# Performance work log

Hardware: AMD Instinct MI355X
Metric: run time of the kernel (lower is better)

Reference implementation:

```python
import jax, jax.numpy as jnp
import numpy as np

N_NODES = 100000


def _gat_conv(x, edge_index, W, att_src, att_dst, bias, concat):
    """PyG-style GATConv (eval mode, self-loops already in edge_index).
    x: [N, F_in], W: [F_in, H*C], att_*: [H, C], bias: [H*C] or [C].
    """
    N = x.shape[0]
    H, C = att_src.shape
    xl = (x @ W).reshape(N, H, C)                      # [N, H, C]
    a_src = jnp.einsum('nhc,hc->nh', xl, att_src)      # [N, H]
    a_dst = jnp.einsum('nhc,hc->nh', xl, att_dst)      # [N, H]
    src, dst = edge_index[0], edge_index[1]
    e = jax.nn.leaky_relu(a_src[src] + a_dst[dst], negative_slope=0.2)  # [E, H]
    # segment softmax over incoming edges per destination node
    e_max = jax.ops.segment_max(e, dst, num_segments=N)                 # [N, H]
    e_exp = jnp.exp(e - e_max[dst])                                     # [E, H]
    denom = jax.ops.segment_sum(e_exp, dst, num_segments=N)             # [N, H]
    alpha = e_exp / (denom[dst] + 1e-16)                                # [E, H]
    msg = xl[src] * alpha[:, :, None]                                   # [E, H, C]
    out = jax.ops.segment_sum(msg, dst, num_segments=N)                 # [N, H, C]
    out = out.reshape(N, H * C) if concat else out.mean(axis=1)
    return out + bias


def setup_inputs() -> dict:
    key = jax.random.key(0)
    ks = jax.random.split(key, 12)
    in_dim, hidden, heads, out_dim = 128, 16, 8, 64
    E = 1600000
    x = jax.random.normal(ks[0], (N_NODES, in_dim), dtype=jnp.float32)
    edge_index = jax.random.randint(ks[1], (2, E), 0, N_NODES, dtype=jnp.int32)
    s1 = 1.0 / np.sqrt(in_dim)
    s2 = 1.0 / np.sqrt(hidden * heads)
    return {
        'x': x,
        'edge_index': edge_index,
        'W1': jax.random.normal(ks[2], (in_dim, heads * hidden), dtype=jnp.float32) * s1,
        'att_src1': jax.random.normal(ks[3], (heads, hidden), dtype=jnp.float32) * 0.1,
        'att_dst1': jax.random.normal(ks[4], (heads, hidden), dtype=jnp.float32) * 0.1,
        'b1': jnp.zeros((heads * hidden,), dtype=jnp.float32),
        'W2': jax.random.normal(ks[5], (heads * hidden, out_dim), dtype=jnp.float32) * s2,
        'att_src2': jax.random.normal(ks[6], (1, out_dim), dtype=jnp.float32) * 0.1,
        'att_dst2': jax.random.normal(ks[7], (1, out_dim), dtype=jnp.float32) * 0.1,
        'b2': jnp.zeros((out_dim,), dtype=jnp.float32),
    }


def reference(x, edge_index, W1, att_src1, att_dst1, b1, W2, att_src2, att_dst2, b2):
    N = x.shape[0]
    # PyG GATConv default add_self_loops=True
    loops = jnp.tile(jnp.arange(N, dtype=edge_index.dtype), (2, 1))
    ei = jnp.concatenate([edge_index, loops], axis=1)
    h = _gat_conv(x, ei, W1, att_src1, att_dst1, b1, concat=True)
    h = jax.nn.elu(h)
    # dropout is identity in eval mode
    out = _gat_conv(h, ei, W2, att_src2, att_dst2, b2, concat=False)
    return out
```

## Files before the change

kernel.cpp:

```cpp
#include <hip/hip_runtime.h>
#include <cmath>

typedef _Float16 half8 __attribute__((ext_vector_type(8)));
typedef float f32x4 __attribute__((ext_vector_type(4)));

#define CAP 48

__device__ __forceinline__ float elu1(float v) {
    return v > 0.f ? v : (__expf(v) - 1.f);
}

__global__ __launch_bounds__(256) void k_gemm1(
    const float* __restrict__ x, const float* __restrict__ W,
    const float* __restrict__ att_s, const float* __restrict__ att_d,
    _Float16* __restrict__ xlh, float* __restrict__ a_s, float* __restrict__ a_d,
    int* __restrict__ cnt, int N)
{
    __shared__ _Float16 Wt[128 * 136];
    int t = threadIdx.x;

    for (int i = blockIdx.x * 256 + t; i < N; i += gridDim.x * 256) cnt[i] = 0;

    for (int i = t; i < 128 * 128; i += 256) {
        int k = i >> 7, n = i & 127;
        Wt[n * 136 + k] = (_Float16)W[i];
    }
    __syncthreads();

    int wave = t >> 6, lane = t & 63;
    int cl = lane & 15, quad = lane >> 4;
    int arow = blockIdx.x * 64 + wave * 16 + cl;
    int rr = arow < N ? arow : N - 1;

    half8 af[4];
#pragma unroll
    for (int ks = 0; ks < 4; ks++) {
        const float4* p = (const float4*)(x + (size_t)rr * 128 + ks * 32 + quad * 8);
        float4 A = p[0], B = p[1];
        af[ks][0] = (_Float16)A.x; af[ks][1] = (_Float16)A.y;
        af[ks][2] = (_Float16)A.z; af[ks][3] = (_Float16)A.w;
        af[ks][4] = (_Float16)B.x; af[ks][5] = (_Float16)B.y;
        af[ks][6] = (_Float16)B.z; af[ks][7] = (_Float16)B.w;
    }

    f32x4 acc[8];
#pragma unroll
    for (int nt = 0; nt < 8; nt++) acc[nt] = (f32x4){0.f, 0.f, 0.f, 0.f};

#pragma unroll
    for (int nt = 0; nt < 8; nt++) {
        int n = nt * 16 + cl;
#pragma unroll
        for (int ks = 0; ks < 4; ks++) {
            half8 bf = *(const half8*)&Wt[n * 136 + ks * 32 + quad * 8];
            acc[nt] = __builtin_amdgcn_mfma_f32_16x16x32_f16(af[ks], bf, acc[nt], 0, 0, 0);
        }
    }

    float asl[8], adl[8];
#pragma unroll
    for (int nt = 0; nt < 8; nt++) {
        asl[nt] = att_s[nt * 16 + cl];
        adl[nt] = att_d[nt * 16 + cl];
    }

    int rbase = blockIdx.x * 64 + wave * 16 + quad * 4;
#pragma unroll
    for (int r = 0; r < 4; r++) {
        int orow = rbase + r;
        bool ok = orow < N;
#pragma unroll
        for (int nt = 0; nt < 8; nt++) {
            float v = acc[nt][r];
            if (ok) xlh[(size_t)orow * 128 + nt * 16 + cl] = (_Float16)v;
        }
#pragma unroll
        for (int nt = 0; nt < 8; nt++) {
            float ps = acc[nt][r] * asl[nt];
            float pd = acc[nt][r] * adl[nt];
            ps += __shfl_xor(ps, 1); ps += __shfl_xor(ps, 2);
            ps += __shfl_xor(ps, 4); ps += __shfl_xor(ps, 8);
            pd += __shfl_xor(pd, 1); pd += __shfl_xor(pd, 2);
            pd += __shfl_xor(pd, 4); pd += __shfl_xor(pd, 8);
            if (ok && cl == 0) {
                a_s[(size_t)orow * 8 + nt] = ps;
                a_d[(size_t)orow * 8 + nt] = pd;
            }
        }
    }
}

__global__ __launch_bounds__(256) void k_scatter(
    const int* __restrict__ src, const int* __restrict__ dst,
    int* __restrict__ cnt, int* __restrict__ sorted, int E, int M, int npc)
{
    int color = blockIdx.x & 7;
    int lo = color * npc, hi = lo + npc;
    int nb = gridDim.x >> 3;
    size_t stride = (size_t)nb * 256;
    for (size_t e = (size_t)(blockIdx.x >> 3) * 256 + threadIdx.x; e < (size_t)M; e += stride) {
        int s, d;
        if (e < (size_t)E) { s = src[e]; d = dst[e]; } else { s = (int)(e - E); d = s; }
        if (d >= lo && d < hi) {
            int pos = atomicAdd(&cnt[d], 1);
            if (pos < CAP) sorted[(size_t)d * CAP + pos] = s;
        }
    }
}

__global__ __launch_bounds__(256) void k_agg1_gemm2(
    const int* __restrict__ cnt, const int* __restrict__ ss,
    const float* __restrict__ as, const float* __restrict__ ad,
    const _Float16* __restrict__ xlh, const float* __restrict__ b1,
    const float* __restrict__ W2,
    const float* __restrict__ att_s2, const float* __restrict__ att_d2,
    _Float16* __restrict__ xl2h, float* __restrict__ a_s2, float* __restrict__ a_d2, int N)
{
    __shared__ _Float16 W2t[64 * 136];
    __shared__ _Float16 Ht[32 * 136];
    __shared__ float asb[2][32], adb[2][32];

    int t = threadIdx.x;

    for (int i = t; i < 128 * 64; i += 256) {
        int k = i >> 6, n = i & 63;
        W2t[n * 136 + k] = (_Float16)W2[i];
    }

    int ln = t >> 3;
    int g = blockIdx.x * 32 + ln;
    int lane8 = t & 7;
    int c = lane8 * 16;
    {
        int gg = g < N ? g : N - 1;
        int deg = cnt[gg]; deg = deg < CAP ? deg : CAP;
        int start = gg * CAP, end = start + deg;
        float adv = ad[(size_t)gg * 8 + lane8];

        float l = 0.f;
        float acc[16];
#pragma unroll
        for (int j = 0; j < 16; j++) acc[j] = 0.f;

        int i = start;
        for (; i + 2 <= end; i += 2) {
            int s0 = ss[i], s1 = ss[i + 1];
            float a0 = as[(size_t)s0 * 8 + lane8];
            float a1 = as[(size_t)s1 * 8 + lane8];
            const _Float16* p0 = xlh + (size_t)s0 * 128 + c;
            const _Float16* p1 = xlh + (size_t)s1 * 128 + c;
            half8 x0a = *(const half8*)p0, x0b = *(const half8*)(p0 + 8);
            half8 x1a = *(const half8*)p1, x1b = *(const half8*)(p1 + 8);
            float v0 = a0 + adv; v0 = v0 > 0.f ? v0 : 0.2f * v0;
            float v1 = a1 + adv; v1 = v1 > 0.f ? v1 : 0.2f * v1;
            float w0 = __expf(v0), w1 = __expf(v1);
            l += w0 + w1;
#pragma unroll
            for (int j = 0; j < 8; j++) {
                acc[j]     += (float)x0a[j] * w0 + (float)x1a[j] * w1;
                acc[j + 8] += (float)x0b[j] * w0 + (float)x1b[j] * w1;
            }
        }
        if (i < end) {
            int s0 = ss[i];
            float v0 = as[(size_t)s0 * 8 + lane8] + adv;
            v0 = v0 > 0.f ? v0 : 0.2f * v0;
            float w0 = __expf(v0);
            l += w0;
            const _Float16* p0 = xlh + (size_t)s0 * 128 + c;
            half8 x0a = *(const half8*)p0, x0b = *(const half8*)(p0 + 8);
#pragma unroll
            for (int j = 0; j < 8; j++) {
                acc[j]     += (float)x0a[j] * w0;
                acc[j + 8] += (float)x0b[j] * w0;
            }
        }
        float inv = 1.f / (l + 1e-16f);
        float4 bq[4];
        bq[0] = *(const float4*)(b1 + c);
        bq[1] = *(const float4*)(b1 + c + 4);
        bq[2] = *(const float4*)(b1 + c + 8);
        bq[3] = *(const float4*)(b1 + c + 12);
        const float* bb = (const float*)bq;
        half8 o0, o1;
#pragma unroll
        for (int j = 0; j < 8; j++) {
            o0[j] = (_Float16)elu1(acc[j] * inv + bb[j]);
            o1[j] = (_Float16)elu1(acc[j + 8] * inv + bb[j + 8]);
        }
        *(half8*)&Ht[ln * 136 + c] = o0;
        *(half8*)&Ht[ln * 136 + c + 8] = o1;
    }
    __syncthreads();

    int wave = t >> 6, lane = t & 63;
    int cl = lane & 15, quad = lane >> 4;
    int rt = wave >> 1;
    int half = wave & 1;

    half8 af[4];
#pragma unroll
    for (int ks = 0; ks < 4; ks++)
        af[ks] = *(const half8*)&Ht[(rt * 16 + cl) * 136 + ks * 32 + quad * 8];

    f32x4 acc2[2];
    acc2[0] = (f32x4){0.f, 0.f, 0.f, 0.f};
    acc2[1] = (f32x4){0.f, 0.f, 0.f, 0.f};
    float asl[2], adl[2];
#pragma unroll
    for (int ntl = 0; ntl < 2; ntl++) {
        int n = (half * 2 + ntl) * 16 + cl;
        asl[ntl] = att_s2[n];
        adl[ntl] = att_d2[n];
#pragma unroll
        for (int ks = 0; ks < 4; ks++) {
            half8 bf = *(const half8*)&W2t[n * 136 + ks * 32 + quad * 8];
            acc2[ntl] = __builtin_amdgcn_mfma_f32_16x16x32_f16(af[ks], bf, acc2[ntl], 0, 0, 0);
        }
    }

#pragma unroll
    for (int r = 0; r < 4; r++) {
        int lrow = rt * 16 + quad * 4 + r;
        int orow = blockIdx.x * 32 + lrow;
        bool ok = orow < N;
        float ps = 0.f, pd = 0.f;
#pragma unroll
        for (int ntl = 0; ntl < 2; ntl++) {
            float v = acc2[ntl][r];
            if (ok) xl2h[(size_t)orow * 64 + (half * 2 + ntl) * 16 + cl] = (_Float16)v;
            ps += v * asl[ntl];
            pd += v * adl[ntl];
        }
        ps += __shfl_xor(ps, 1); ps += __shfl_xor(ps, 2);
        ps += __shfl_xor(ps, 4); ps += __shfl_xor(ps, 8);
        pd += __shfl_xor(pd, 1); pd += __shfl_xor(pd, 2);
        pd += __shfl_xor(pd, 4); pd += __shfl_xor(pd, 8);
        if (cl == 0) { asb[half][lrow] = ps; adb[half][lrow] = pd; }
    }
    __syncthreads();
    if (t < 32) {
        int orow = blockIdx.x * 32 + t;
        if (orow < N) {
            a_s2[orow] = asb[0][t] + asb[1][t];
            a_d2[orow] = adb[0][t] + adb[1][t];
        }
    }
}

__global__ __launch_bounds__(256) void k_agg2(
    const int* __restrict__ cnt, const int* __restrict__ ss,
    const float* __restrict__ as, const float* __restrict__ ad,
    const _Float16* __restrict__ xlh, const float* __restrict__ b2,
    float* __restrict__ out, int N)
{
    int t = threadIdx.x;
    int g = (blockIdx.x * 256 + t) >> 3;
    if (g >= N) return;
    int lane = t & 7;
    int c = lane * 8;
    int deg = cnt[g]; deg = deg < CAP ? deg : CAP;
    int start = g * CAP, end = start + deg;
    float adv = ad[g];

    float l = 0.f;
    float acc[8];
#pragma unroll
    for (int j = 0; j < 8; j++) acc[j] = 0.f;

    int i = start;
    for (; i + 4 <= end; i += 4) {
        int s0 = ss[i], s1 = ss[i + 1], s2 = ss[i + 2], s3 = ss[i + 3];
        float a0 = as[s0], a1 = as[s1], a2 = as[s2], a3 = as[s3];
        half8 x0 = *(const half8*)(xlh + (size_t)s0 * 64 + c);
        half8 x1 = *(const half8*)(xlh + (size_t)s1 * 64 + c);
        half8 x2 = *(const half8*)(xlh + (size_t)s2 * 64 + c);
        half8 x3 = *(const half8*)(xlh + (size_t)s3 * 64 + c);
        float v0 = a0 + adv; v0 = v0 > 0.f ? v0 : 0.2f * v0;
        float v1 = a1 + adv; v1 = v1 > 0.f ? v1 : 0.2f * v1;
        float v2 = a2 + adv; v2 = v2 > 0.f ? v2 : 0.2f * v2;
        float v3 = a3 + adv; v3 = v3 > 0.f ? v3 : 0.2f * v3;
        float w0 = __expf(v0), w1 = __expf(v1), w2 = __expf(v2), w3 = __expf(v3);
        l += (w0 + w1) + (w2 + w3);
#pragma unroll
        for (int j = 0; j < 8; j++)
            acc[j] += ((float)x0[j] * w0 + (float)x1[j] * w1)
                    + ((float)x2[j] * w2 + (float)x3[j] * w3);
    }
    for (; i < end; i++) {
        int s0 = ss[i];
        float v0 = as[s0] + adv;
        v0 = v0 > 0.f ? v0 : 0.2f * v0;
        float w0 = __expf(v0);
        l += w0;
        half8 x0 = *(const half8*)(xlh + (size_t)s0 * 64 + c);
#pragma unroll
        for (int j = 0; j < 8; j++) acc[j] += (float)x0[j] * w0;
    }
    float inv = 1.f / (l + 1e-16f);
    float4 b0 = *(const float4*)(b2 + c);
    float4 b4 = *(const float4*)(b2 + c + 4);
    float bb[8] = {b0.x, b0.y, b0.z, b0.w, b4.x, b4.y, b4.z, b4.w};
    float4 o0, o1;
    o0.x = acc[0] * inv + bb[0];
    o0.y = acc[1] * inv + bb[1];
    o0.z = acc[2] * inv + bb[2];
    o0.w = acc[3] * inv + bb[3];
    o1.x = acc[4] * inv + bb[4];
    o1.y = acc[5] * inv + bb[5];
    o1.z = acc[6] * inv + bb[6];
    o1.w = acc[7] * inv + bb[7];
    *(float4*)(out + (size_t)g * 64 + c) = o0;
    *(float4*)(out + (size_t)g * 64 + c + 4) = o1;
}

extern "C" void kernel_launch(void* const* d_in, const int* in_sizes, int n_in,
                              void* d_out, int out_size, void* d_ws, size_t ws_size,
                              hipStream_t stream) {
    const float* x   = (const float*)d_in[0];
    const int*   ei  = (const int*)  d_in[1];
    const float* W1  = (const float*)d_in[2];
    const float* as1 = (const float*)d_in[3];
    const float* ad1 = (const float*)d_in[4];
    const float* b1  = (const float*)d_in[5];
    const float* W2  = (const float*)d_in[6];
    const float* as2 = (const float*)d_in[7];
    const float* ad2 = (const float*)d_in[8];
    const float* b2  = (const float*)d_in[9];

    const int N = in_sizes[0] / 128;
    const int E = in_sizes[1] / 2;
    const int M = E + N;
    const int npc = (N + 7) / 8;
    const int SB = ((M + 256 * 8 - 1) / (256 * 8)) * 8;
    const int* src = ei;
    const int* dst = ei + E;

    float* ws    = (float*)d_ws;
    _Float16* xl1h = (_Float16*)ws;
    float* as1v  = ws   + (size_t)N * 64;
    float* ad1v  = as1v + (size_t)N * 8;
    _Float16* xl2h = (_Float16*)(ad1v + (size_t)N * 8);
    float* as2v  = ad1v + (size_t)N * 8 + (size_t)N * 32;
    float* ad2v  = as2v + (size_t)N;
    int*   cnt   = (int*)(ad2v + (size_t)N);
    int*   sorted= cnt + (size_t)N;
    float* out   = (float*)d_out;

    size_t need = ((size_t)N * (115 + CAP)) * 4;
    if (ws_size < need) return;

    k_gemm1  <<<(N + 63) / 64, 256, 0, stream>>>(x, W1, as1, ad1, xl1h, as1v, ad1v, cnt, N);
    k_scatter<<<SB, 256, 0, stream>>>(src, dst, cnt, sorted, E, M, npc);

    k_agg1_gemm2<<<(N + 31) / 32, 256, 0, stream>>>(
        cnt, sorted, as1v, ad1v, xl1h, b1, W2, as2, ad2, xl2h, as2v, ad2v, N);

    k_agg2 <<<(int)(((size_t)N * 8 + 255) / 256), 256, 0, stream>>>(
        cnt, sorted, as2v, ad2v, xl2h, b2, out, N);
}
```

Before: 343.8 us.

## Fuse edge scatter and layer-1 GEMM into one heterogeneous kernel launch

Merges the CSR-bucket scatter and the first GEMM into a single launch: the first SB blocks do the atomic edge scatter and the rest do the MFMA projection, so the two independent phases can run concurrently on the GPU. The cnt zeroing moves out of the GEMM into a hipMemsetAsync so the scatter's atomics no longer depend on it. The shared W tile shrinks to half (loaded in two K-halves) to cut LDS use and raise occupancy alongside the scatter blocks. This adds a memset launch and an extra barrier plus a second W load per GEMM block.

```diff
diff --git a/kernel.cpp b/kernel.cpp
--- a/kernel.cpp
+++ b/kernel.cpp
@@ -10,26 +10,36 @@
     return v > 0.f ? v : (__expf(v) - 1.f);
 }
 
-__global__ __launch_bounds__(256) void k_gemm1(
+__global__ __launch_bounds__(256) void k_build(
+    const int* __restrict__ src, const int* __restrict__ dst,
+    int* __restrict__ cnt, int* __restrict__ sorted, int E, int M, int npc, int SB,
     const float* __restrict__ x, const float* __restrict__ W,
     const float* __restrict__ att_s, const float* __restrict__ att_d,
-    _Float16* __restrict__ xlh, float* __restrict__ a_s, float* __restrict__ a_d,
-    int* __restrict__ cnt, int N)
+    _Float16* __restrict__ xlh, float* __restrict__ a_s, float* __restrict__ a_d, int N)
 {
-    __shared__ _Float16 Wt[128 * 136];
+    __shared__ _Float16 Wt[128 * 72];
     int t = threadIdx.x;
 
-    for (int i = blockIdx.x * 256 + t; i < N; i += gridDim.x * 256) cnt[i] = 0;
-
-    for (int i = t; i < 128 * 128; i += 256) {
-        int k = i >> 7, n = i & 127;
-        Wt[n * 136 + k] = (_Float16)W[i];
-    }
-    __syncthreads();
-
+    if ((int)blockIdx.x < SB) {
+        int color = blockIdx.x & 7;
+        int lo = color * npc, hi = lo + npc;
+        int nb = SB >> 3;
+        size_t stride = (size_t)nb * 256;
+        for (size_t e = (size_t)(blockIdx.x >> 3) * 256 + t; e < (size_t)M; e += stride) {
+            int s, d;
+            if (e < (size_t)E) { s = src[e]; d = dst[e]; } else { s = (int)(e - E); d = s; }
+            if (d >= lo && d < hi) {
+                int pos = atomicAdd(&cnt[d], 1);
+                if (pos < CAP) sorted[(size_t)d * CAP + pos] = s;
+            }
+        }
+        return;
+    }
+
+    int bx = blockIdx.x - SB;
     int wave = t >> 6, lane = t & 63;
     int cl = lane & 15, quad = lane >> 4;
-    int arow = blockIdx.x * 64 + wave * 16 + cl;
+    int arow = bx * 64 + wave * 16 + cl;
     int rr = arow < N ? arow : N - 1;
 
     half8 af[4];
@@ -48,12 +58,22 @@
     for (int nt = 0; nt < 8; nt++) acc[nt] = (f32x4){0.f, 0.f, 0.f, 0.f};
 
 #pragma unroll
-    for (int nt = 0; nt < 8; nt++) {
-        int n = nt * 16 + cl;
-#pragma unroll
-        for (int ks = 0; ks < 4; ks++) {
-            half8 bf = *(const half8*)&Wt[n * 136 + ks * 32 + quad * 8];
-            acc[nt] = __builtin_amdgcn_mfma_f32_16x16x32_f16(af[ks], bf, acc[nt], 0, 0, 0);
+    for (int h = 0; h < 2; h++) {
+        if (h) __syncthreads();
+        for (int i = t; i < 128 * 64; i += 256) {
+            int k0 = i >> 7, n = i & 127;
+            Wt[n * 72 + k0] = (_Float16)W[(size_t)(h * 64 + k0) * 128 + n];
+        }
+        __syncthreads();
+#pragma unroll
+        for (int nt = 0; nt < 8; nt++) {
+            int n = nt * 16 + cl;
+#pragma unroll
+            for (int ks2 = 0; ks2 < 2; ks2++) {
+                half8 bf = *(const half8*)&Wt[n * 72 + ks2 * 32 + quad * 8];
+                acc[nt] = __builtin_amdgcn_mfma_f32_16x16x32_f16(
+                    af[h * 2 + ks2], bf, acc[nt], 0, 0, 0);
+            }
         }
     }
 
@@ -64,7 +84,7 @@
         adl[nt] = att_d[nt * 16 + cl];
     }
 
-    int rbase = blockIdx.x * 64 + wave * 16 + quad * 4;
+    int rbase = bx * 64 + wave * 16 + quad * 4;
 #pragma unroll
     for (int r = 0; r < 4; r++) {
         int orow = rbase + r;
@@ -86,24 +106,6 @@
                 a_s[(size_t)orow * 8 + nt] = ps;
                 a_d[(size_t)orow * 8 + nt] = pd;
             }
-        }
-    }
-}
-
-__global__ __launch_bounds__(256) void k_scatter(
-    const int* __restrict__ src, const int* __restrict__ dst,
-    int* __restrict__ cnt, int* __restrict__ sorted, int E, int M, int npc)
-{
-    int color = blockIdx.x & 7;
-    int lo = color * npc, hi = lo + npc;
-    int nb = gridDim.x >> 3;
-    size_t stride = (size_t)nb * 256;
-    for (size_t e = (size_t)(blockIdx.x >> 3) * 256 + threadIdx.x; e < (size_t)M; e += stride) {
-        int s, d;
-        if (e < (size_t)E) { s = src[e]; d = dst[e]; } else { s = (int)(e - E); d = s; }
-        if (d >= lo && d < hi) {
-            int pos = atomicAdd(&cnt[d], 1);
-            if (pos < CAP) sorted[(size_t)d * CAP + pos] = s;
         }
     }
 }
@@ -333,6 +335,7 @@
     const int M = E + N;
     const int npc = (N + 7) / 8;
     const int SB = ((M + 256 * 8 - 1) / (256 * 8)) * 8;
+    const int GB = (N + 63) / 64;
     const int* src = ei;
     const int* dst = ei + E;
 
@@ -350,8 +353,11 @@
     size_t need = ((size_t)N * (115 + CAP)) * 4;
     if (ws_size < need) return;
 
-    k_gemm1  <<<(N + 63) / 64, 256, 0, stream>>>(x, W1, as1, ad1, xl1h, as1v, ad1v, cnt, N);
-    k_scatter<<<SB, 256, 0, stream>>>(src, dst, cnt, sorted, E, M, npc);
+    hipMemsetAsync(cnt, 0, (size_t)N * 4, stream);
+
+    k_build<<<SB + GB, 256, 0, stream>>>(
+        src, dst, cnt, sorted, E, M, npc, SB,
+        x, W1, as1, ad1, xl1h, as1v, ad1v, N);
 
     k_agg1_gemm2<<<(N + 31) / 32, 256, 0, stream>>>(
         cnt, sorted, as1v, ad1v, xl1h, b1, W2, as2, ad2, xl2h, as2v, ad2v, N);
```

Measured after the change: 335.4 us. -2.4%, faster.
